# Kernel tuning notes

Hardware: AMD Instinct MI355X
Metric: run time of the kernel (lower is better)

Reference implementation:

```python
import jax, jax.numpy as jnp
import numpy as np

INPUT_SIZE = 300
HIDDEN = 16


def setup_inputs() -> dict:
    key = jax.random.key(0)
    ks = jax.random.split(key, 9)
    T, B = 512, 512
    s_ih = 1.0 / np.sqrt(HIDDEN)
    inp = {
        "x": jax.random.normal(ks[0], (T, B, INPUT_SIZE), dtype=jnp.float32),
        # LSTMCell params (torch gate order: i, f, g, o)
        "W_ih": jax.random.uniform(ks[1], (4 * HIDDEN, INPUT_SIZE), jnp.float32, -s_ih, s_ih),
        "W_hh": jax.random.uniform(ks[2], (4 * HIDDEN, HIDDEN), jnp.float32, -s_ih, s_ih),
        "b_ih": jax.random.uniform(ks[3], (4 * HIDDEN,), jnp.float32, -s_ih, s_ih),
        "b_hh": jax.random.uniform(ks[4], (4 * HIDDEN,), jnp.float32, -s_ih, s_ih),
        # MLP head
        "W1": jax.random.uniform(ks[5], (64, HIDDEN), jnp.float32, -s_ih, s_ih),
        "b1": jax.random.uniform(ks[6], (64,), jnp.float32, -s_ih, s_ih),
        "W2": jax.random.uniform(ks[7], (1, 64), jnp.float32, -0.125, 0.125),
        "b2": jax.random.uniform(ks[8], (1,), jnp.float32, -0.125, 0.125),
    }
    return inp


def _lstm_final_h(x, W_ih, W_hh, b_ih, b_hh):
    B = x.shape[1]
    h0 = jnp.zeros((B, HIDDEN), dtype=x.dtype)
    c0 = jnp.zeros((B, HIDDEN), dtype=x.dtype)
    # precompute input projections for all timesteps: [T, B, 4H]
    xg = jnp.einsum("tbi,gi->tbg", x, W_ih) + b_ih + b_hh

    def step(carry, xg_t):
        h, c = carry
        gates = xg_t + h @ W_hh.T  # [B, 4H]
        i, f, g, o = jnp.split(gates, 4, axis=-1)
        c = jax.nn.sigmoid(f) * c + jax.nn.sigmoid(i) * jnp.tanh(g)
        h = jax.nn.sigmoid(o) * jnp.tanh(c)
        return (h, c), None

    (h, _), _ = jax.lax.scan(step, (h0, c0), xg)
    return h  # [B, HIDDEN]


def reference(x, W_ih, W_hh, b_ih, b_hh, W1, b1, W2, b2):
    h = _lstm_final_h(x, W_ih, W_hh, b_ih, b_hh)
    # eval mode: dropout is identity
    z = jax.nn.relu(h @ W1.T + b1)
    out = 4.0 * jax.nn.sigmoid(z @ W2.T + b2)
    return out.squeeze(-1)  # [B]
```

## Files before the change

kernel.cpp:

```cpp
#include <hip/hip_runtime.h>
#include <hip/hip_bf16.h>


#define T_STEPS 512
#define BATCH   512
#define K_IN    300
#define NG      64
#define HID     16
#define CHUNK   16

typedef float  f32x4  __attribute__((ext_vector_type(4)));
typedef float  f32x8  __attribute__((ext_vector_type(8)));
typedef __bf16 bf16x8 __attribute__((ext_vector_type(8)));

static __device__ __forceinline__ bf16x8 cvt8(float4 lo, float4 hi) {
    f32x8 t;
    t[0] = lo.x; t[1] = lo.y; t[2] = lo.z; t[3] = lo.w;
    t[4] = hi.x; t[5] = hi.y; t[6] = hi.z; t[7] = hi.w;
    return __builtin_convertvector(t, bf16x8);
}

__global__ __launch_bounds__(256) void xg_gemm(
    const float* __restrict__ x,
    const float* __restrict__ W,
    const float* __restrict__ b_ih,
    const float* __restrict__ b_hh,
    float* __restrict__ xg)
{
    __shared__ __align__(16) __bf16 Wl[40 * 512];

    const int lane = threadIdx.x & 63;
    const int wv   = threadIdx.x >> 6;
    const int m16  = lane & 15;
    const int quad = lane >> 4;
    const int row0 = blockIdx.x * 64 + wv * 16;
    const float4 z4 = {0.f, 0.f, 0.f, 0.f};

    const float* xr = x + (size_t)(row0 + m16) * K_IN;

    float4 alo[10], ahi[10];
#pragma unroll
    for (int ks = 0; ks < 10; ++ks) {
        const int k = ks * 32 + quad * 8;
        alo[ks] = (k + 3 < K_IN) ? *(const float4*)(xr + k)     : z4;
        ahi[ks] = (k + 7 < K_IN) ? *(const float4*)(xr + k + 4) : z4;
    }

    {
        const float* wrow = W + (size_t)(wv * 16 + m16) * K_IN;
#pragma unroll
        for (int ks = 0; ks < 10; ++ks) {
            const int k = ks * 32 + quad * 8;
            const float4 lo = (k + 3 < K_IN) ? *(const float4*)(wrow + k)     : z4;
            const float4 hi = (k + 7 < K_IN) ? *(const float4*)(wrow + k + 4) : z4;
            *(bf16x8*)&Wl[(ks * 4 + wv) * 512 + lane * 8] = cvt8(lo, hi);
        }
    }
    __syncthreads();

    f32x4 acc[4];
#pragma unroll
    for (int nt = 0; nt < 4; ++nt) acc[nt] = (f32x4){0.f, 0.f, 0.f, 0.f};

#pragma unroll
    for (int ks = 0; ks < 10; ++ks) {
        const bf16x8 af = cvt8(alo[ks], ahi[ks]);
#pragma unroll
        for (int nt = 0; nt < 4; ++nt) {
            const bf16x8 bf = *(const bf16x8*)&Wl[(ks * 4 + nt) * 512 + lane * 8];
            acc[nt] = __builtin_amdgcn_mfma_f32_16x16x32_bf16(af, bf, acc[nt], 0, 0, 0);
        }
    }

    float bias[4];
#pragma unroll
    for (int nt = 0; nt < 4; ++nt)
        bias[nt] = b_ih[nt * 16 + m16] + b_hh[nt * 16 + m16];

#pragma unroll
    for (int reg = 0; reg < 4; ++reg) {
        const int R = row0 + quad * 4 + reg;
        const int t = R >> 9;
        const int b = R & (BATCH - 1);
        float4 o;
        o.x = acc[0][reg] + bias[0];
        o.y = acc[1][reg] + bias[1];
        o.z = acc[2][reg] + bias[2];
        o.w = acc[3][reg] + bias[3];
        *(float4*)(xg + ((size_t)b * T_STEPS + t) * NG + m16 * 4) = o;
    }
}

__global__ __launch_bounds__(64) void lstm_scan(
    const float* __restrict__ xg,
    const float* __restrict__ Whh,
    const float* __restrict__ W1,
    const float* __restrict__ b1,
    const float* __restrict__ W2,
    const float* __restrict__ b2,
    float* __restrict__ out)
{
    __shared__ __align__(16) float xs[2][CHUNK][NG];

    const int lane  = threadIdx.x;
    const int j     = lane & 15;
    const int qd    = lane >> 4;
    const int batch = blockIdx.x;
    const int perm  = j * 4 + qd;

    float w[HID];
#pragma unroll
    for (int k = 0; k < HID; k += 4)
        *(float4*)&w[k] = *(const float4*)(Whh + lane * HID + k);

    const float kk = (qd == 2) ? -2.f : -1.f;
    const float mm = (qd == 2) ?  2.f :  1.f;
    const float nn = (qd == 2) ? -1.f :  0.f;

    const int aI = 4 * j, aF = 4 * (16 + j), aG = 4 * (32 + j), aO = 4 * (48 + j);

    const float* xb = xg + (size_t)batch * T_STEPS * NG;

#pragma unroll
    for (int q = 0; q < 4; ++q)
        *(float4*)((float*)xs + q * 256 + lane * 4) =
            *(const float4*)(xb + q * 256 + lane * 4);

    float c = 0.f;
    float hs[HID];
#pragma unroll
    for (int k = 0; k < HID; ++k) hs[k] = 0.f;

#pragma unroll 1
    for (int ci = 0; ci < T_STEPS / CHUNK; ++ci) {
        const int cur = ci & 1;

        float4 nx0, nx1, nx2, nx3;
        if (ci < T_STEPS / CHUNK - 1) {
            const float* src = xb + (size_t)(ci + 1) * CHUNK * NG;
            nx0 = *(const float4*)(src +   0 + lane * 4);
            nx1 = *(const float4*)(src + 256 + lane * 4);
            nx2 = *(const float4*)(src + 512 + lane * 4);
            nx3 = *(const float4*)(src + 768 + lane * 4);
        }

        const float* bp = (const float*)xs + cur * (CHUNK * NG) + perm;

#pragma unroll
        for (int tin = 0; tin < CHUNK; ++tin) {
            const float pre = bp[tin * NG];

            float p0 = pre, p1 = 0.f, p2 = 0.f, p3 = 0.f;
#pragma unroll
            for (int k = 0; k < 4; ++k) {
                p0 = fmaf(w[k],      hs[k],      p0);
                p1 = fmaf(w[k + 4],  hs[k + 4],  p1);
                p2 = fmaf(w[k + 8],  hs[k + 8],  p2);
                p3 = fmaf(w[k + 12], hs[k + 12], p3);
            }
            const float s = (p0 + p1) + (p2 + p3);

            const float a   = __builtin_amdgcn_rcpf(1.f + __expf(kk * s));
            const float act = fmaf(a, mm, nn);

            const int av = __float_as_int(act);
            const float ai = __int_as_float(__builtin_amdgcn_ds_bpermute(aI, av));
            const float af = __int_as_float(__builtin_amdgcn_ds_bpermute(aF, av));
            const float ag = __int_as_float(__builtin_amdgcn_ds_bpermute(aG, av));
            const float ao = __int_as_float(__builtin_amdgcn_ds_bpermute(aO, av));

            c = fmaf(af, c, ai * ag);
            const float th = fmaf(2.f, __builtin_amdgcn_rcpf(1.f + __expf(-2.f * c)), -1.f);
            const float h  = ao * th;

            const int hI = __float_as_int(h);
#pragma unroll
            for (int k = 0; k < HID; ++k)
                hs[k] = __int_as_float(__builtin_amdgcn_readlane(hI, k));
        }

        if (ci < T_STEPS / CHUNK - 1) {
            float* wp = (float*)xs + (cur ^ 1) * (CHUNK * NG) + lane * 4;
            *(float4*)(wp +   0) = nx0;
            *(float4*)(wp + 256) = nx1;
            *(float4*)(wp + 512) = nx2;
            *(float4*)(wp + 768) = nx3;
        }
    }

    float z = b1[lane];
#pragma unroll
    for (int k = 0; k < HID; ++k)
        z = fmaf(W1[lane * HID + k], hs[k], z);
    z = fmaxf(z, 0.f);
    float y = z * W2[lane];

#pragma unroll
    for (int m = 1; m < 64; m <<= 1) y += __shfl_xor(y, m, 64);

    if (lane == 0)
        out[batch] = 4.f * __builtin_amdgcn_rcpf(1.f + __expf(-(y + b2[0])));
}

extern "C" void kernel_launch(void* const* d_in, const int* in_sizes, int n_in,
                              void* d_out, int out_size, void* d_ws, size_t ws_size,
                              hipStream_t stream) {
    const float* x    = (const float*)d_in[0];
    const float* W_ih = (const float*)d_in[1];
    const float* W_hh = (const float*)d_in[2];
    const float* b_ih = (const float*)d_in[3];
    const float* b_hh = (const float*)d_in[4];
    const float* W1   = (const float*)d_in[5];
    const float* b1   = (const float*)d_in[6];
    const float* W2   = (const float*)d_in[7];
    const float* b2   = (const float*)d_in[8];
    float* out = (float*)d_out;
    float* xg  = (float*)d_ws;

    xg_gemm<<<dim3(T_STEPS * BATCH / 64), dim3(256), 0, stream>>>(x, W_ih, b_ih, b_hh, xg);
    lstm_scan<<<dim3(BATCH), dim3(64), 0, stream>>>(xg, W_hh, W1, b1, W2, b2, out);
}
```

Baseline: 529.2 us.

## Fuse input-projection GEMM into LSTM scan kernel with per-chunk MFMA

Merges the separate xg GEMM kernel into the recurrent scan kernel. Each 64-thread block now loads its own batch column of x for the next 16 timesteps, computes the gate pre-activations with bf16 MFMA while the current chunk is scanned, and stages them through padded shared memory. This removes the xg workspace write and readback and the second kernel launch. In exchange, each of the 512 single-wave blocks reads x with strided, poorly coalesced accesses and carries the GEMM work on the latency-bound scan path, which the surrounding code only partly hides.

```diff
diff --git a/kernel.cpp b/kernel.cpp
--- a/kernel.cpp
+++ b/kernel.cpp
@@ -8,6 +8,7 @@
 #define NG      64
 #define HID     16
 #define CHUNK   16
+#define NCHUNK  (T_STEPS / CHUNK)
 
 typedef float  f32x4  __attribute__((ext_vector_type(4)));
 typedef float  f32x8  __attribute__((ext_vector_type(8)));
@@ -20,79 +21,11 @@
     return __builtin_convertvector(t, bf16x8);
 }
 
-__global__ __launch_bounds__(256) void xg_gemm(
+__global__ __launch_bounds__(64) void lstm_fused(
     const float* __restrict__ x,
     const float* __restrict__ W,
     const float* __restrict__ b_ih,
     const float* __restrict__ b_hh,
-    float* __restrict__ xg)
-{
-    __shared__ __align__(16) __bf16 Wl[40 * 512];
-
-    const int lane = threadIdx.x & 63;
-    const int wv   = threadIdx.x >> 6;
-    const int m16  = lane & 15;
-    const int quad = lane >> 4;
-    const int row0 = blockIdx.x * 64 + wv * 16;
-    const float4 z4 = {0.f, 0.f, 0.f, 0.f};
-
-    const float* xr = x + (size_t)(row0 + m16) * K_IN;
-
-    float4 alo[10], ahi[10];
-#pragma unroll
-    for (int ks = 0; ks < 10; ++ks) {
-        const int k = ks * 32 + quad * 8;
-        alo[ks] = (k + 3 < K_IN) ? *(const float4*)(xr + k)     : z4;
-        ahi[ks] = (k + 7 < K_IN) ? *(const float4*)(xr + k + 4) : z4;
-    }
-
-    {
-        const float* wrow = W + (size_t)(wv * 16 + m16) * K_IN;
-#pragma unroll
-        for (int ks = 0; ks < 10; ++ks) {
-            const int k = ks * 32 + quad * 8;
-            const float4 lo = (k + 3 < K_IN) ? *(const float4*)(wrow + k)     : z4;
-            const float4 hi = (k + 7 < K_IN) ? *(const float4*)(wrow + k + 4) : z4;
-            *(bf16x8*)&Wl[(ks * 4 + wv) * 512 + lane * 8] = cvt8(lo, hi);
-        }
-    }
-    __syncthreads();
-
-    f32x4 acc[4];
-#pragma unroll
-    for (int nt = 0; nt < 4; ++nt) acc[nt] = (f32x4){0.f, 0.f, 0.f, 0.f};
-
-#pragma unroll
-    for (int ks = 0; ks < 10; ++ks) {
-        const bf16x8 af = cvt8(alo[ks], ahi[ks]);
-#pragma unroll
-        for (int nt = 0; nt < 4; ++nt) {
-            const bf16x8 bf = *(const bf16x8*)&Wl[(ks * 4 + nt) * 512 + lane * 8];
-            acc[nt] = __builtin_amdgcn_mfma_f32_16x16x32_bf16(af, bf, acc[nt], 0, 0, 0);
-        }
-    }
-
-    float bias[4];
-#pragma unroll
-    for (int nt = 0; nt < 4; ++nt)
-        bias[nt] = b_ih[nt * 16 + m16] + b_hh[nt * 16 + m16];
-
-#pragma unroll
-    for (int reg = 0; reg < 4; ++reg) {
-        const int R = row0 + quad * 4 + reg;
-        const int t = R >> 9;
-        const int b = R & (BATCH - 1);
-        float4 o;
-        o.x = acc[0][reg] + bias[0];
-        o.y = acc[1][reg] + bias[1];
-        o.z = acc[2][reg] + bias[2];
-        o.w = acc[3][reg] + bias[3];
-        *(float4*)(xg + ((size_t)b * T_STEPS + t) * NG + m16 * 4) = o;
-    }
-}
-
-__global__ __launch_bounds__(64) void lstm_scan(
-    const float* __restrict__ xg,
     const float* __restrict__ Whh,
     const float* __restrict__ W1,
     const float* __restrict__ b1,
@@ -100,55 +33,96 @@
     const float* __restrict__ b2,
     float* __restrict__ out)
 {
-    __shared__ __align__(16) float xs[2][CHUNK][NG];
+    __shared__ __align__(16) __bf16 Wl[40 * 512];
+    __shared__ float xs[NG * 17];
 
     const int lane  = threadIdx.x;
-    const int j     = lane & 15;
-    const int qd    = lane >> 4;
+    const int m16   = lane & 15;
+    const int quad  = lane >> 4;
     const int batch = blockIdx.x;
-    const int perm  = j * 4 + qd;
+    const float4 z4 = {0.f, 0.f, 0.f, 0.f};
+
+    float4 alo[10], ahi[10];
+    {
+        const float* xr = x + ((size_t)m16 * BATCH + batch) * K_IN;
+#pragma unroll
+        for (int ks = 0; ks < 10; ++ks) {
+            const int k = ks * 32 + quad * 8;
+            alo[ks] = (k + 3 < K_IN) ? *(const float4*)(xr + k)     : z4;
+            ahi[ks] = (k + 7 < K_IN) ? *(const float4*)(xr + k + 4) : z4;
+        }
+    }
+
+#pragma unroll
+    for (int nt = 0; nt < 4; ++nt) {
+        const float* wrow = W + (size_t)(nt * 16 + m16) * K_IN;
+#pragma unroll
+        for (int ks = 0; ks < 10; ++ks) {
+            const int k = ks * 32 + quad * 8;
+            const float4 lo = (k + 3 < K_IN) ? *(const float4*)(wrow + k)     : z4;
+            const float4 hi = (k + 7 < K_IN) ? *(const float4*)(wrow + k + 4) : z4;
+            *(bf16x8*)&Wl[(ks * 4 + nt) * 512 + lane * 8] = cvt8(lo, hi);
+        }
+    }
 
     float w[HID];
 #pragma unroll
     for (int k = 0; k < HID; k += 4)
         *(float4*)&w[k] = *(const float4*)(Whh + lane * HID + k);
 
-    const float kk = (qd == 2) ? -2.f : -1.f;
-    const float mm = (qd == 2) ?  2.f :  1.f;
-    const float nn = (qd == 2) ? -1.f :  0.f;
-
-    const int aI = 4 * j, aF = 4 * (16 + j), aG = 4 * (32 + j), aO = 4 * (48 + j);
-
-    const float* xb = xg + (size_t)batch * T_STEPS * NG;
-
-#pragma unroll
-    for (int q = 0; q < 4; ++q)
-        *(float4*)((float*)xs + q * 256 + lane * 4) =
-            *(const float4*)(xb + q * 256 + lane * 4);
+    const float kk = (quad == 2) ? -2.f : -1.f;
+    const float mm = (quad == 2) ?  2.f :  1.f;
+    const float nn = (quad == 2) ? -1.f :  0.f;
+    const int aI = 4 * m16, aF = 4 * (16 + m16),
+              aG = 4 * (32 + m16), aO = 4 * (48 + m16);
+
+    float bias[4];
+#pragma unroll
+    for (int nt = 0; nt < 4; ++nt)
+        bias[nt] = b_ih[nt * 16 + m16] + b_hh[nt * 16 + m16];
 
     float c = 0.f;
     float hs[HID];
 #pragma unroll
     for (int k = 0; k < HID; ++k) hs[k] = 0.f;
 
+    f32x4 acc[4];
+#pragma unroll
+    for (int nt = 0; nt < 4; ++nt) acc[nt] = (f32x4){0.f, 0.f, 0.f, 0.f};
+#pragma unroll
+    for (int ks = 0; ks < 10; ++ks) {
+        const bf16x8 af = cvt8(alo[ks], ahi[ks]);
+#pragma unroll
+        for (int nt = 0; nt < 4; ++nt)
+            acc[nt] = __builtin_amdgcn_mfma_f32_16x16x32_bf16(
+                af, *(const bf16x8*)&Wl[(ks * 4 + nt) * 512 + lane * 8],
+                acc[nt], 0, 0, 0);
+    }
+
 #pragma unroll 1
-    for (int ci = 0; ci < T_STEPS / CHUNK; ++ci) {
-        const int cur = ci & 1;
-
-        float4 nx0, nx1, nx2, nx3;
-        if (ci < T_STEPS / CHUNK - 1) {
-            const float* src = xb + (size_t)(ci + 1) * CHUNK * NG;
-            nx0 = *(const float4*)(src +   0 + lane * 4);
-            nx1 = *(const float4*)(src + 256 + lane * 4);
-            nx2 = *(const float4*)(src + 512 + lane * 4);
-            nx3 = *(const float4*)(src + 768 + lane * 4);
-        }
-
-        const float* bp = (const float*)xs + cur * (CHUNK * NG) + perm;
+    for (int ci = 0; ci < NCHUNK; ++ci) {
+        if (ci + 1 < NCHUNK) {
+            const float* xr =
+                x + ((size_t)((ci + 1) * CHUNK + m16) * BATCH + batch) * K_IN;
+#pragma unroll
+            for (int ks = 0; ks < 10; ++ks) {
+                const int k = ks * 32 + quad * 8;
+                alo[ks] = (k + 3 < K_IN) ? *(const float4*)(xr + k)     : z4;
+                ahi[ks] = (k + 7 < K_IN) ? *(const float4*)(xr + k + 4) : z4;
+            }
+        }
+
+#pragma unroll
+        for (int nt = 0; nt < 4; ++nt)
+#pragma unroll
+            for (int reg = 0; reg < 4; ++reg)
+                xs[(nt * 16 + m16) * 17 + quad * 4 + reg] = acc[nt][reg] + bias[nt];
+
+        asm volatile("" ::: "memory");
 
 #pragma unroll
         for (int tin = 0; tin < CHUNK; ++tin) {
-            const float pre = bp[tin * NG];
+            const float pre = xs[lane * 17 + tin];
 
             float p0 = pre, p1 = 0.f, p2 = 0.f, p3 = 0.f;
 #pragma unroll
@@ -164,14 +138,14 @@
             const float act = fmaf(a, mm, nn);
 
             const int av = __float_as_int(act);
-            const float ai = __int_as_float(__builtin_amdgcn_ds_bpermute(aI, av));
-            const float af = __int_as_float(__builtin_amdgcn_ds_bpermute(aF, av));
-            const float ag = __int_as_float(__builtin_amdgcn_ds_bpermute(aG, av));
-            const float ao = __int_as_float(__builtin_amdgcn_ds_bpermute(aO, av));
-
-            c = fmaf(af, c, ai * ag);
+            const float gi = __int_as_float(__builtin_amdgcn_ds_bpermute(aI, av));
+            const float gf = __int_as_float(__builtin_amdgcn_ds_bpermute(aF, av));
+            const float gg = __int_as_float(__builtin_amdgcn_ds_bpermute(aG, av));
+            const float go = __int_as_float(__builtin_amdgcn_ds_bpermute(aO, av));
+
+            c = fmaf(gf, c, gi * gg);
             const float th = fmaf(2.f, __builtin_amdgcn_rcpf(1.f + __expf(-2.f * c)), -1.f);
-            const float h  = ao * th;
+            const float h  = go * th;
 
             const int hI = __float_as_int(h);
 #pragma unroll
@@ -179,12 +153,20 @@
                 hs[k] = __int_as_float(__builtin_amdgcn_readlane(hI, k));
         }
 
-        if (ci < T_STEPS / CHUNK - 1) {
-            float* wp = (float*)xs + (cur ^ 1) * (CHUNK * NG) + lane * 4;
-            *(float4*)(wp +   0) = nx0;
-            *(float4*)(wp + 256) = nx1;
-            *(float4*)(wp + 512) = nx2;
-            *(float4*)(wp + 768) = nx3;
+        asm volatile("" ::: "memory");
+
+        if (ci + 1 < NCHUNK) {
+#pragma unroll
+            for (int nt = 0; nt < 4; ++nt) acc[nt] = (f32x4){0.f, 0.f, 0.f, 0.f};
+#pragma unroll
+            for (int ks = 0; ks < 10; ++ks) {
+                const bf16x8 af = cvt8(alo[ks], ahi[ks]);
+#pragma unroll
+                for (int nt = 0; nt < 4; ++nt)
+                    acc[nt] = __builtin_amdgcn_mfma_f32_16x16x32_bf16(
+                        af, *(const bf16x8*)&Wl[(ks * 4 + nt) * 512 + lane * 8],
+                        acc[nt], 0, 0, 0);
+            }
         }
     }
 
@@ -215,8 +197,8 @@
     const float* W2   = (const float*)d_in[7];
     const float* b2   = (const float*)d_in[8];
     float* out = (float*)d_out;
-    float* xg  = (float*)d_ws;
-
-    xg_gemm<<<dim3(T_STEPS * BATCH / 64), dim3(256), 0, stream>>>(x, W_ih, b_ih, b_hh, xg);
-    lstm_scan<<<dim3(BATCH), dim3(64), 0, stream>>>(xg, W_hh, W1, b1, W2, b2, out);
+    (void)d_ws; (void)ws_size;
+
+    lstm_fused<<<dim3(BATCH), dim3(64), 0, stream>>>(
+        x, W_ih, b_ih, b_hh, W_hh, W1, b1, W2, b2, out);
 }
```

Result: slower. 593.8 us (+12.2%).
